# Performance work log

Measured on AMD Instinct MI355X. Metric: run time of the kernel, lower is better.

The kernel has to match this reference:

```python
import jax, jax.numpy as jnp
import numpy as np


def setup_inputs() -> dict:
    key = jax.random.key(0)
    k1, k2 = jax.random.split(key)
    n, m, d = 8192, 8192, 64
    x = jax.random.normal(k1, (n, d), dtype=jnp.float32)
    y = jax.random.normal(k2, (m, d), dtype=jnp.float32)
    gamma = jnp.ones((), dtype=jnp.float32)  # learnable bandwidth, init_gamma=1.0
    return {"x": x, "y": y, "gamma": gamma}


def reference(x, y, gamma):
    # RBF kernel: exp(-gamma * ||x_i - y_j||^2), computed via the
    x_sq = jnp.sum(x * x, axis=-1, keepdims=True)          # (n, 1)
    y_sq = jnp.sum(y * y, axis=-1, keepdims=True).T        # (1, m)
    xy = x @ y.T                                           # (n, m) GEMM
    sq_dist = jnp.maximum(x_sq + y_sq - 2.0 * xy, 0.0)     # clamp fp error
    return jnp.exp(-gamma * sq_dist)                       # (n, m)
```

## Files before the change

kernel.cpp:

```cpp
#include <hip/hip_runtime.h>
#include <hip/hip_bf16.h>


#define DD 64
#define BM 128
#define BN 128
#define IPB 4

typedef __attribute__((ext_vector_type(8))) short short8;
typedef __attribute__((ext_vector_type(4))) float f32x4;

#if __has_builtin(__builtin_amdgcn_exp2f)
#define EXP2(x) __builtin_amdgcn_exp2f(x)
#else
#define EXP2(x) exp2f(x)
#endif

__device__ __forceinline__ unsigned short f2bf_rne(float f) {
  unsigned u = __float_as_uint(f);
  unsigned r = u + 0x7FFFu + ((u >> 16) & 1u);
  return (unsigned short)(r >> 16);
}

__device__ __forceinline__ long fidx(int p, int s, int rb) {
  return ((((long)p * 2 + s) * 8) + rb) * 64;
}

__global__ __launch_bounds__(256)
void prep_mix2(const float* __restrict__ X, const float* __restrict__ Y,
               short8* __restrict__ XHf, short8* __restrict__ XLf,
               unsigned short* __restrict__ YHg, unsigned short* __restrict__ YLg,
               float* __restrict__ xsq, float* __restrict__ ysq, int n) {
  int t = blockIdx.x * 256 + threadIdx.x;
  int row_g = t >> 3;
  int chunk = t & 7;
  int isX = (row_g < n);
  int r = isX ? row_g : row_g - n;
  const float* src = (isX ? X : Y) + (long)r * DD + chunk * 8;
  float4 v0 = ((const float4*)src)[0];
  float4 v1 = ((const float4*)src)[1];
  float f[8] = {v0.x, v0.y, v0.z, v0.w, v1.x, v1.y, v1.z, v1.w};

  short8 h8, l8;
  float ss = 0.f;
#pragma unroll
  for (int q = 0; q < 8; ++q) {
    unsigned short h = f2bf_rne(f[q]);
    float hv = __uint_as_float(((unsigned)h) << 16);
    h8[q] = (short)h;
    l8[q] = (short)f2bf_rne(f[q] - hv);
    ss = fmaf(f[q], f[q], ss);
  }
  if (isX) {
    int pn = r >> 7, rb = (r >> 4) & 7, lr = r & 15;
    int s = chunk >> 2, hg = chunk & 3;
    long o = fidx(pn, s, rb) + hg * 16 + lr;
    XHf[o] = h8;
    XLf[o] = l8;
  } else {
    int sw = (chunk * 16) ^ ((r & 7) << 4);
    *(short8*)((char*)YHg + (long)r * 128 + sw) = h8;
    *(short8*)((char*)YLg + (long)r * 128 + sw) = l8;
  }
  ss += __shfl_xor(ss, 1);
  ss += __shfl_xor(ss, 2);
  ss += __shfl_xor(ss, 4);
  if (chunk == 0) (isX ? xsq : ysq)[r] = ss;
}

__global__ __launch_bounds__(256, 2)
void rbf_isweep(const short8* __restrict__ XHf, const short8* __restrict__ XLf,
                const unsigned short* __restrict__ YHg, const unsigned short* __restrict__ YLg,
                const float* __restrict__ gptr,
                const float* __restrict__ xsq, const float* __restrict__ ysq,
                float* __restrict__ Out, int mcols) {
  __shared__ __align__(128) char lds[65536];

  const int tid = threadIdx.x;
  const int lane = tid & 63;
  const int wid = tid >> 6;
  const int ig0 = blockIdx.y * IPB;
  const long j0 = (long)blockIdx.x * (2 * BN);

  const char* srcs[4] = {(const char*)YHg + j0 * 128,        (const char*)YLg + j0 * 128,
                         (const char*)YHg + (j0 + BN) * 128, (const char*)YLg + (j0 + BN) * 128};
#pragma unroll
  for (int t4 = 0; t4 < 4; ++t4) {
#pragma unroll
    for (int it = 0; it < 4; ++it) {
      int off = it * 4096 + wid * 1024;
      __builtin_amdgcn_global_load_lds(
          (const __attribute__((address_space(1))) void*)(srcs[t4] + off + lane * 16),
          (__attribute__((address_space(3))) void*)(lds + t4 * 16384 + off),
          16, 0, 0);
    }
  }

  const int wr = wid >> 1, wc = wid & 1;
  const int lr = lane & 15;
  const int hg = lane >> 4;

  short8 afh[2][4], afl[2][4];
#pragma unroll
  for (int s = 0; s < 2; ++s)
#pragma unroll
    for (int q = 0; q < 4; ++q) {
      afh[s][q] = XHf[fidx(ig0, s, wr * 4 + q) + lane];
      afl[s][q] = XLf[fidx(ig0, s, wr * 4 + q) + lane];
    }

  const float g = *gptr;
  const float cf = -g * 1.4426950408889634f;
  const float nc2 = -2.0f * cf;

  __syncthreads();

  for (int p = 0; p < IPB; ++p) {
    const int ip = ig0 + p;
    const long i0 = (long)ip * BM;
    float cxr[4];
#pragma unroll
    for (int m2 = 0; m2 < 4; ++m2) cxr[m2] = cf * xsq[i0 + wr * 64 + m2 * 16 + lr];

#pragma unroll
    for (int t = 0; t < 2; ++t) {
      const long jt = j0 + (long)t * BN;
      const int yb = t * 32768;

      short8 bfh[2][4], bfl[2][4];
#pragma unroll
      for (int s = 0; s < 2; ++s)
#pragma unroll
        for (int q = 0; q < 4; ++q) {
          int rb = wc * 64 + q * 16 + lr;
          int ob = (s * 64 + hg * 16) ^ ((rb & 7) << 4);
          bfh[s][q] = *(const short8*)(lds + yb + rb * 128 + ob);
          bfl[s][q] = *(const short8*)(lds + yb + 16384 + rb * 128 + ob);
        }

      float4 cyv[4];
#pragma unroll
      for (int n2 = 0; n2 < 4; ++n2) {
        float4 yq = *(const float4*)&ysq[jt + wc * 64 + n2 * 16 + hg * 4];
        cyv[n2] = make_float4(cf * yq.x, cf * yq.y, cf * yq.z, cf * yq.w);
      }

#pragma unroll
      for (int m2 = 0; m2 < 4; ++m2) {
        long row = i0 + wr * 64 + m2 * 16 + lr;
        float* op = Out + row * (long)mcols + jt + wc * 64 + hg * 4;
#pragma unroll
        for (int n2 = 0; n2 < 4; ++n2) {
          f32x4 a = (f32x4){0.f, 0.f, 0.f, 0.f};
#pragma unroll
          for (int s = 0; s < 2; ++s) {
            a = __builtin_amdgcn_mfma_f32_16x16x32_bf16(bfh[s][n2], afh[s][m2], a, 0, 0, 0);
            a = __builtin_amdgcn_mfma_f32_16x16x32_bf16(bfh[s][n2], afl[s][m2], a, 0, 0, 0);
            a = __builtin_amdgcn_mfma_f32_16x16x32_bf16(bfl[s][n2], afh[s][m2], a, 0, 0, 0);
          }
          float o[4];
          o[0] = EXP2(fminf(fmaf(nc2, a[0], cxr[m2] + cyv[n2].x), 0.f));
          o[1] = EXP2(fminf(fmaf(nc2, a[1], cxr[m2] + cyv[n2].y), 0.f));
          o[2] = EXP2(fminf(fmaf(nc2, a[2], cxr[m2] + cyv[n2].z), 0.f));
          o[3] = EXP2(fminf(fmaf(nc2, a[3], cxr[m2] + cyv[n2].w), 0.f));
          *(float4*)(op + n2 * 16) = *(float4*)o;
          __builtin_amdgcn_sched_barrier(0);
        }
      }
    }

    if (p + 1 < IPB) {
#pragma unroll
      for (int s = 0; s < 2; ++s)
#pragma unroll
        for (int q = 0; q < 4; ++q) {
          afh[s][q] = XHf[fidx(ip + 1, s, wr * 4 + q) + lane];
          afl[s][q] = XLf[fidx(ip + 1, s, wr * 4 + q) + lane];
        }
    }
  }
}

__global__ __launch_bounds__(256)
void prep_sq(const float* __restrict__ X, const float* __restrict__ Y,
             float* __restrict__ xsq, float* __restrict__ ysq, int n) {
  int t = blockIdx.x * 256 + threadIdx.x;
  int row = t >> 4;
  int c = t & 15;
  const float* src;
  float* dst;
  if (row < n) { src = X + (long)row * DD; dst = xsq + row; }
  else         { src = Y + (long)(row - n) * DD; dst = ysq + (row - n); }
  float4 v = ((const float4*)src)[c];
  float s = v.x * v.x + v.y * v.y + v.z * v.z + v.w * v.w;
  s += __shfl_xor(s, 1);
  s += __shfl_xor(s, 2);
  s += __shfl_xor(s, 4);
  s += __shfl_xor(s, 8);
  if (c == 0) *dst = s;
}

__global__ __launch_bounds__(256, 2)
void rbf_mfma_fb(const float* __restrict__ X, const float* __restrict__ Y,
                 const float* __restrict__ gptr,
                 const float* __restrict__ xsq, const float* __restrict__ ysq,
                 float* __restrict__ Out, int mcols) {
  __shared__ unsigned short XH[128 * DD], XL[128 * DD];
  __shared__ unsigned short YH[128 * DD], YL[128 * DD];
  const int tid = threadIdx.x;
  const long i0 = (long)blockIdx.y * 128;
  const long j0 = (long)blockIdx.x * 128;
#pragma unroll
  for (int it = 0; it < 16; ++it) {
    int e = it * 256 + tid;
    int half = e >> 11;
    int idx = e & 2047;
    int row = idx >> 4;
    int c4 = idx & 15;
    const float* src = half ? (Y + (j0 + row) * DD) : (X + (i0 + row) * DD);
    float4 v = ((const float4*)src)[c4];
    float f[4] = {v.x, v.y, v.z, v.w};
    unsigned short h[4], l[4];
#pragma unroll
    for (int q = 0; q < 4; ++q) {
      h[q] = f2bf_rne(f[q]);
      float hv = __uint_as_float(((unsigned)h[q]) << 16);
      l[q] = f2bf_rne(f[q] - hv);
    }
    int sw = (c4 * 8) ^ ((row & 7) << 4);
    unsigned short* Ht = half ? YH : XH;
    unsigned short* Lt = half ? YL : XL;
    *(ushort4*)((char*)Ht + row * 128 + sw) = make_ushort4(h[0], h[1], h[2], h[3]);
    *(ushort4*)((char*)Lt + row * 128 + sw) = make_ushort4(l[0], l[1], l[2], l[3]);
  }
  __syncthreads();
  const int lane = tid & 63;
  const int wid = tid >> 6;
  const int wr = wid >> 1, wc = wid & 1;
  const int lr = lane & 15;
  const int hg = lane >> 4;
  f32x4 acc[4][4];
#pragma unroll
  for (int a = 0; a < 4; ++a)
#pragma unroll
    for (int c = 0; c < 4; ++c) acc[a][c] = (f32x4){0.f, 0.f, 0.f, 0.f};
  const unsigned short* At[3] = {XH, XL, XH};
  const unsigned short* Bt[3] = {YH, YH, YL};
#pragma unroll
  for (int p = 0; p < 3; ++p) {
#pragma unroll
    for (int s = 0; s < 2; ++s) {
      const int kbyte = s * 64 + hg * 16;
      short8 af[4], bfv[4];
#pragma unroll
      for (int m2 = 0; m2 < 4; ++m2) {
        int row = wr * 64 + m2 * 16 + lr;
        af[m2] = *(const short8*)((const char*)At[p] + row * 128 + (kbyte ^ ((row & 7) << 4)));
      }
#pragma unroll
      for (int n2 = 0; n2 < 4; ++n2) {
        int row = wc * 64 + n2 * 16 + lr;
        bfv[n2] = *(const short8*)((const char*)Bt[p] + row * 128 + (kbyte ^ ((row & 7) << 4)));
      }
#pragma unroll
      for (int m2 = 0; m2 < 4; ++m2)
#pragma unroll
        for (int n2 = 0; n2 < 4; ++n2)
          acc[m2][n2] = __builtin_amdgcn_mfma_f32_16x16x32_bf16(af[m2], bfv[n2], acc[m2][n2], 0, 0, 0);
    }
  }
  const float g = *gptr;
  float yv[4];
#pragma unroll
  for (int n2 = 0; n2 < 4; ++n2) yv[n2] = ysq[j0 + wc * 64 + n2 * 16 + lr];
#pragma unroll
  for (int m2 = 0; m2 < 4; ++m2) {
#pragma unroll
    for (int j = 0; j < 4; ++j) {
      long row = i0 + wr * 64 + m2 * 16 + hg * 4 + j;
      float xr = xsq[row];
      float* op = Out + row * (long)mcols + j0 + wc * 64 + lr;
#pragma unroll
      for (int n2 = 0; n2 < 4; ++n2) {
        float d = fmaxf(xr + yv[n2] - 2.0f * acc[m2][n2][j], 0.f);
        op[n2 * 16] = __expf(-g * d);
      }
    }
  }
}

extern "C" void kernel_launch(void* const* d_in, const int* in_sizes, int n_in,
                              void* d_out, int out_size, void* d_ws, size_t ws_size,
                              hipStream_t stream) {
  const float* x = (const float*)d_in[0];
  const float* y = (const float*)d_in[1];
  const float* g = (const float*)d_in[2];
  float* out = (float*)d_out;

  const int n = in_sizes[0] / DD;
  const int m = in_sizes[1] / DD;

  const size_t split_bytes = (size_t)(n + m) * DD * 2 * sizeof(unsigned short);
  const size_t needed = split_bytes + (size_t)(n + m) * sizeof(float);

  if (ws_size >= needed && (n % (BM * IPB)) == 0 && (m % (2 * BN)) == 0) {
    short8* XHf = (short8*)d_ws;
    short8* XLf = XHf + (size_t)n * DD / 8;
    unsigned short* YHg = (unsigned short*)(XLf + (size_t)n * DD / 8);
    unsigned short* YLg = YHg + (size_t)m * DD;
    float* xsq = (float*)(YLg + (size_t)m * DD);
    float* ysq = xsq + n;
    prep_mix2<<<(n + m) * 8 / 256, 256, 0, stream>>>(x, y, XHf, XLf, YHg, YLg, xsq, ysq, n);
    dim3 grid(m / (2 * BN), n / (BM * IPB));
    rbf_isweep<<<grid, 256, 0, stream>>>(XHf, XLf, YHg, YLg, g, xsq, ysq, out, m);
  } else {
    float* xsq = (float*)d_ws;
    float* ysq = xsq + n;
    prep_sq<<<(n + m) / 16, 256, 0, stream>>>(x, y, xsq, ysq, n);
    dim3 grid2(m / 128, n / 128);
    rbf_mfma_fb<<<grid2, 256, 0, stream>>>(x, y, g, xsq, ysq, out, m);
  }
}
```

Baseline: 52.18 us.

## Halve per-block Y tile and load B fragments per column to raise occupancy

Each block now covers one 128-column Y tile instead of two, so LDS use drops from 64KB to 32KB and launch bounds rise from 2 to 4 blocks per CU. The loop order changes so that each n2 column's B fragments are read from LDS just before use, which lowers the register footprint compared with holding all four. The aim is more waves resident to hide memory latency during a store-bound exp write-out. In exchange the grid doubles, X fragments are reloaded by twice as many blocks, and the output store order becomes less contiguous per row.

```diff
diff --git a/kernel.cpp b/kernel.cpp
--- a/kernel.cpp
+++ b/kernel.cpp
@@ -68,29 +68,28 @@
   if (chunk == 0) (isX ? xsq : ysq)[r] = ss;
 }
 
-__global__ __launch_bounds__(256, 2)
-void rbf_isweep(const short8* __restrict__ XHf, const short8* __restrict__ XLf,
-                const unsigned short* __restrict__ YHg, const unsigned short* __restrict__ YLg,
-                const float* __restrict__ gptr,
-                const float* __restrict__ xsq, const float* __restrict__ ysq,
-                float* __restrict__ Out, int mcols) {
-  __shared__ __align__(128) char lds[65536];
+__global__ __launch_bounds__(256, 4)
+void rbf_w16(const short8* __restrict__ XHf, const short8* __restrict__ XLf,
+             const unsigned short* __restrict__ YHg, const unsigned short* __restrict__ YLg,
+             const float* __restrict__ gptr,
+             const float* __restrict__ xsq, const float* __restrict__ ysq,
+             float* __restrict__ Out, int mcols) {
+  __shared__ __align__(128) char lds[32768];
 
   const int tid = threadIdx.x;
   const int lane = tid & 63;
   const int wid = tid >> 6;
   const int ig0 = blockIdx.y * IPB;
-  const long j0 = (long)blockIdx.x * (2 * BN);
-
-  const char* srcs[4] = {(const char*)YHg + j0 * 128,        (const char*)YLg + j0 * 128,
-                         (const char*)YHg + (j0 + BN) * 128, (const char*)YLg + (j0 + BN) * 128};
-#pragma unroll
-  for (int t4 = 0; t4 < 4; ++t4) {
+  const long j0 = (long)blockIdx.x * BN;
+
+#pragma unroll
+  for (int t4 = 0; t4 < 2; ++t4) {
+    const char* src = (t4 ? (const char*)YLg : (const char*)YHg) + j0 * 128;
 #pragma unroll
     for (int it = 0; it < 4; ++it) {
       int off = it * 4096 + wid * 1024;
       __builtin_amdgcn_global_load_lds(
-          (const __attribute__((address_space(1))) void*)(srcs[t4] + off + lane * 16),
+          (const __attribute__((address_space(1))) void*)(src + off + lane * 16),
           (__attribute__((address_space(3))) void*)(lds + t4 * 16384 + off),
           16, 0, 0);
     }
@@ -123,49 +122,36 @@
     for (int m2 = 0; m2 < 4; ++m2) cxr[m2] = cf * xsq[i0 + wr * 64 + m2 * 16 + lr];
 
 #pragma unroll
-    for (int t = 0; t < 2; ++t) {
-      const long jt = j0 + (long)t * BN;
-      const int yb = t * 32768;
-
-      short8 bfh[2][4], bfl[2][4];
-#pragma unroll
-      for (int s = 0; s < 2; ++s)
-#pragma unroll
-        for (int q = 0; q < 4; ++q) {
-          int rb = wc * 64 + q * 16 + lr;
-          int ob = (s * 64 + hg * 16) ^ ((rb & 7) << 4);
-          bfh[s][q] = *(const short8*)(lds + yb + rb * 128 + ob);
-          bfl[s][q] = *(const short8*)(lds + yb + 16384 + rb * 128 + ob);
+    for (int n2 = 0; n2 < 4; ++n2) {
+      short8 bfh[2], bfl[2];
+#pragma unroll
+      for (int s = 0; s < 2; ++s) {
+        int rb = wc * 64 + n2 * 16 + lr;
+        int ob = (s * 64 + hg * 16) ^ ((rb & 7) << 4);
+        bfh[s] = *(const short8*)(lds + rb * 128 + ob);
+        bfl[s] = *(const short8*)(lds + 16384 + rb * 128 + ob);
+      }
+      float4 yq = *(const float4*)&ysq[j0 + wc * 64 + n2 * 16 + hg * 4];
+      float cy[4] = {cf * yq.x, cf * yq.y, cf * yq.z, cf * yq.w};
+
+#pragma unroll
+      for (int m2 = 0; m2 < 4; ++m2) {
+        f32x4 a = (f32x4){0.f, 0.f, 0.f, 0.f};
+#pragma unroll
+        for (int s = 0; s < 2; ++s) {
+          a = __builtin_amdgcn_mfma_f32_16x16x32_bf16(bfh[s], afh[s][m2], a, 0, 0, 0);
+          a = __builtin_amdgcn_mfma_f32_16x16x32_bf16(bfh[s], afl[s][m2], a, 0, 0, 0);
+          a = __builtin_amdgcn_mfma_f32_16x16x32_bf16(bfl[s], afh[s][m2], a, 0, 0, 0);
         }
-
-      float4 cyv[4];
-#pragma unroll
-      for (int n2 = 0; n2 < 4; ++n2) {
-        float4 yq = *(const float4*)&ysq[jt + wc * 64 + n2 * 16 + hg * 4];
-        cyv[n2] = make_float4(cf * yq.x, cf * yq.y, cf * yq.z, cf * yq.w);
-      }
-
-#pragma unroll
-      for (int m2 = 0; m2 < 4; ++m2) {
         long row = i0 + wr * 64 + m2 * 16 + lr;
-        float* op = Out + row * (long)mcols + jt + wc * 64 + hg * 4;
-#pragma unroll
-        for (int n2 = 0; n2 < 4; ++n2) {
-          f32x4 a = (f32x4){0.f, 0.f, 0.f, 0.f};
-#pragma unroll
-          for (int s = 0; s < 2; ++s) {
-            a = __builtin_amdgcn_mfma_f32_16x16x32_bf16(bfh[s][n2], afh[s][m2], a, 0, 0, 0);
-            a = __builtin_amdgcn_mfma_f32_16x16x32_bf16(bfh[s][n2], afl[s][m2], a, 0, 0, 0);
-            a = __builtin_amdgcn_mfma_f32_16x16x32_bf16(bfl[s][n2], afh[s][m2], a, 0, 0, 0);
-          }
-          float o[4];
-          o[0] = EXP2(fminf(fmaf(nc2, a[0], cxr[m2] + cyv[n2].x), 0.f));
-          o[1] = EXP2(fminf(fmaf(nc2, a[1], cxr[m2] + cyv[n2].y), 0.f));
-          o[2] = EXP2(fminf(fmaf(nc2, a[2], cxr[m2] + cyv[n2].z), 0.f));
-          o[3] = EXP2(fminf(fmaf(nc2, a[3], cxr[m2] + cyv[n2].w), 0.f));
-          *(float4*)(op + n2 * 16) = *(float4*)o;
-          __builtin_amdgcn_sched_barrier(0);
-        }
+        float* op = Out + row * (long)mcols + j0 + wc * 64 + n2 * 16 + hg * 4;
+        float o[4];
+        o[0] = EXP2(fminf(fmaf(nc2, a[0], cxr[m2] + cy[0]), 0.f));
+        o[1] = EXP2(fminf(fmaf(nc2, a[1], cxr[m2] + cy[1]), 0.f));
+        o[2] = EXP2(fminf(fmaf(nc2, a[2], cxr[m2] + cy[2]), 0.f));
+        o[3] = EXP2(fminf(fmaf(nc2, a[3], cxr[m2] + cy[3]), 0.f));
+        *(float4*)op = *(float4*)o;
+        __builtin_amdgcn_sched_barrier(0);
       }
     }
 
@@ -303,7 +289,7 @@
   const size_t split_bytes = (size_t)(n + m) * DD * 2 * sizeof(unsigned short);
   const size_t needed = split_bytes + (size_t)(n + m) * sizeof(float);
 
-  if (ws_size >= needed && (n % (BM * IPB)) == 0 && (m % (2 * BN)) == 0) {
+  if (ws_size >= needed && (n % (BM * IPB)) == 0 && (m % BN) == 0) {
     short8* XHf = (short8*)d_ws;
     short8* XLf = XHf + (size_t)n * DD / 8;
     unsigned short* YHg = (unsigned short*)(XLf + (size_t)n * DD / 8);
@@ -311,8 +297,8 @@
     float* xsq = (float*)(YLg + (size_t)m * DD);
     float* ysq = xsq + n;
     prep_mix2<<<(n + m) * 8 / 256, 256, 0, stream>>>(x, y, XHf, XLf, YHg, YLg, xsq, ysq, n);
-    dim3 grid(m / (2 * BN), n / (BM * IPB));
-    rbf_isweep<<<grid, 256, 0, stream>>>(XHf, XLf, YHg, YLg, g, xsq, ysq, out, m);
+    dim3 grid(m / BN, n / (BM * IPB));
+    rbf_w16<<<grid, 256, 0, stream>>>(XHf, XLf, YHg, YLg, g, xsq, ysq, out, m);
   } else {
     float* xsq = (float*)d_ws;
     float* ysq = xsq + n;
```

Measured after the change: 59.71 us. 1.14x slower.
